# Optimization experiments

Measured on AMD Instinct MI355X. Metric: run time of the kernel, lower is better.

The kernel has to match this reference:

```python
import jax, jax.numpy as jnp
import numpy as np

EMBED_DIM = 768
NUM_HEADS = 12
HEAD_DIM = EMBED_DIM // NUM_HEADS
SCALE = HEAD_DIM ** -0.5


def setup_inputs() -> dict:
    key = jax.random.key(0)
    k_x, k_qkv, k_proj, k_pb = jax.random.split(key, 4)
    x = jax.random.normal(k_x, (2, 4096, EMBED_DIM), dtype=jnp.float32)
    # nn.Linear weights stored as [out, in]; qkv_bias=False -> no qkv bias
    W_qkv = jax.random.normal(k_qkv, (3 * EMBED_DIM, EMBED_DIM), dtype=jnp.float32) * (EMBED_DIM ** -0.5)
    W_proj = jax.random.normal(k_proj, (EMBED_DIM, EMBED_DIM), dtype=jnp.float32) * (EMBED_DIM ** -0.5)
    b_proj = jax.random.normal(k_pb, (EMBED_DIM,), dtype=jnp.float32) * 0.01
    return {"x": x, "W_qkv": W_qkv, "W_proj": W_proj, "b_proj": b_proj}


def reference(x, W_qkv, W_proj, b_proj):
    bs, seq_len, _ = x.shape
    qkv = jnp.einsum("bse,fe->bsf", x, W_qkv)  # [B,S,3E]
    q, k, v = jnp.split(qkv, 3, axis=-1)
    # [B,S,E] -> [B,H,S,D]
    def to_heads(t):
        return t.reshape(bs, seq_len, NUM_HEADS, HEAD_DIM).transpose(0, 2, 1, 3)
    q, k, v = to_heads(q), to_heads(k), to_heads(v)
    scores = jnp.einsum("bhqd,bhkd->bhqk", q, k) * SCALE
    attn = jax.nn.softmax(scores, axis=-1)  # dropout p=0.0 -> identity
    out = jnp.einsum("bhqk,bhkd->bhqd", attn, v)
    out = out.transpose(0, 2, 1, 3).reshape(bs, seq_len, EMBED_DIM)
    return jnp.einsum("bse,fe->bsf", out, W_proj) + b_proj
```

## Files before the change

kernel.cpp:

```cpp
#include <hip/hip_runtime.h>
#include <stdint.h>


typedef unsigned short u16;
typedef __attribute__((ext_vector_type(8))) short short8;
typedef __attribute__((ext_vector_type(4))) float float4v;

#define C2F 0.18033688011112042f

#if __has_builtin(__builtin_amdgcn_exp2f)
#define QSCALE C2F
#define FEXP(x) __builtin_amdgcn_exp2f(x)
#else
#define QSCALE 0.125f
#define FEXP(x) __expf(x)
#endif

__device__ __forceinline__ u16 f2bf(float f) {
  uint32_t u = __float_as_uint(f);
  u += 0x7FFFu + ((u >> 16) & 1u);
  return (u16)(u >> 16);
}
__device__ __forceinline__ float4v mfma16(short8 a, short8 b, float4v c) {
  return __builtin_amdgcn_mfma_f32_16x16x32_bf16(a, b, c, 0, 0, 0);
}
__device__ __forceinline__ short8 ld8(const u16* p) { return *(const short8*)p; }
__device__ __forceinline__ void st8(u16* p, short8 v) { *(short8*)p = v; }

__device__ __forceinline__ void dma16(const u16* g, u16* l) {
  __builtin_amdgcn_global_load_lds(
      (const __attribute__((address_space(1))) void*)g,
      (__attribute__((address_space(3))) void*)l, 16, 0, 0);
}

__device__ __forceinline__ uint32_t pk2(float lo, float hi) {
  return __builtin_amdgcn_perm(__float_as_uint(hi) + 0x8000u,
                               __float_as_uint(lo) + 0x8000u, 0x07060302u);
}
__device__ __forceinline__ short8 pack8(float4 a, float4 b) {
  union { short8 s; uint32_t u[4]; } r;
  r.u[0] = pk2(a.x, a.y); r.u[1] = pk2(a.z, a.w);
  r.u[2] = pk2(b.x, b.y); r.u[3] = pk2(b.z, b.w);
  return r.s;
}

__global__ __launch_bounds__(256, 3) void k_gemm_qkv(
    const float* __restrict__ x, const float* __restrict__ Wq,
    u16* __restrict__ qkv2, u16* __restrict__ Vt) {
  __shared__ u16 sA[128 * 64];
  __shared__ u16 sB[128 * 64];
  const int m0 = blockIdx.x * 128;
  const int f0 = blockIdx.y * 128;
  const bool vmode = (f0 >= 1536);
  const int tid = threadIdx.x;
  const int w = tid >> 6, lane = tid & 63;
  const int quad = lane >> 4, r = lane & 15;
  const int srow = lane >> 3, sc = lane & 7;

  float4v acc[4][4];
#pragma unroll
  for (int i = 0; i < 4; ++i)
#pragma unroll
    for (int j = 0; j < 4; ++j) acc[i][j] = (float4v){0.f, 0.f, 0.f, 0.f};

  float4 px[4][2], pw[4][2];
#pragma unroll
  for (int t = 0; t < 4; ++t) {
    const int row = 32 * w + 8 * t + srow;
    const float4* xa = (const float4*)x + (size_t)(m0 + row) * 192 + 2 * sc;
    const float4* wa = (const float4*)Wq + (size_t)(f0 + row) * 192 + 2 * sc;
    px[t][0] = xa[0]; px[t][1] = xa[1];
    pw[t][0] = wa[0]; pw[t][1] = wa[1];
  }

  for (int kt = 0; kt < 12; ++kt) {
#pragma unroll
    for (int t = 0; t < 4; ++t) {
      const int row = 32 * w + 8 * t + srow;
      st8(sA + row * 64 + 8 * (sc ^ srow), pack8(px[t][0], px[t][1]));
      st8(sB + row * 64 + 8 * (sc ^ srow), pack8(pw[t][0], pw[t][1]));
    }
    __syncthreads();
    if (kt + 1 < 12) {
#pragma unroll
      for (int t = 0; t < 4; ++t) {
        const int row = 32 * w + 8 * t + srow;
        const float4* xa = (const float4*)x + (size_t)(m0 + row) * 192 + (kt + 1) * 16 + 2 * sc;
        const float4* wa = (const float4*)Wq + (size_t)(f0 + row) * 192 + (kt + 1) * 16 + 2 * sc;
        px[t][0] = xa[0]; px[t][1] = xa[1];
        pw[t][0] = wa[0]; pw[t][1] = wa[1];
      }
    }
    const u16* At = vmode ? sB : sA;
    const u16* Bt = vmode ? sA : sB;
#pragma unroll
    for (int ks = 0; ks < 2; ++ks) {
      short8 a[4], b[4];
#pragma unroll
      for (int i = 0; i < 4; ++i) {
        const int ra = 64 * (w >> 1) + 16 * i + r;
        const int rb = 64 * (w & 1) + 16 * i + r;
        a[i] = ld8(At + ra * 64 + 8 * ((4 * ks + quad) ^ (ra & 7)));
        b[i] = ld8(Bt + rb * 64 + 8 * ((4 * ks + quad) ^ (rb & 7)));
      }
#pragma unroll
      for (int mi = 0; mi < 4; ++mi)
#pragma unroll
        for (int nf = 0; nf < 4; ++nf) acc[mi][nf] = mfma16(a[mi], b[nf], acc[mi][nf]);
    }
    __syncthreads();
  }

  if (!vmode) {
    const float qs = (f0 < 768) ? QSCALE : 1.0f;
#pragma unroll
    for (int mi = 0; mi < 4; ++mi) {
      const int m = m0 + 64 * (w >> 1) + 16 * mi + 4 * quad;
#pragma unroll
      for (int nf = 0; nf < 4; ++nf) {
        const int f = f0 + 64 * (w & 1) + 16 * nf + r;
#pragma unroll
        for (int reg = 0; reg < 4; ++reg)
          qkv2[(size_t)(m + reg) * 1536 + f] = f2bf(acc[mi][nf][reg] * qs);
      }
    }
  } else {
#pragma unroll
    for (int mi = 0; mi < 4; ++mi) {
      const int vcol = f0 - 1536 + 64 * (w >> 1) + 16 * mi + 4 * quad;
#pragma unroll
      for (int nf = 0; nf < 4; ++nf) {
        const int m = m0 + 64 * (w & 1) + 16 * nf + r;
        const int mp = (m & ~0x1C) | ((m & 0x0C) << 1) | ((m & 0x10) >> 2);
#pragma unroll
        for (int reg = 0; reg < 4; ++reg)
          Vt[(size_t)(vcol + reg) * 8192 + mp] = f2bf(acc[mi][nf][reg]);
      }
    }
  }
}

__global__ __launch_bounds__(512, 6) void k_flash(
    const u16* __restrict__ qkv2, const u16* __restrict__ Vt, u16* __restrict__ attn) {
  __shared__ u16 sK[2][64 * 64];
  __shared__ u16 sV[2][64 * 64];
  const int id = blockIdx.x;
  const int xcd = id & 7, slot = id >> 3;
  const int bh = xcd * 3 + (slot >> 5);
  const int qt = slot & 31;
  const int b = bh / 12, h = bh % 12;
  const int tid = threadIdx.x;
  const int w = tid >> 6, lane = tid & 63;
  const int quad = lane >> 4, r = lane & 15;
  const int srow = lane >> 3, sc = lane & 7;
  const u16* Qg = qkv2 + (size_t)b * 4096 * 1536 + h * 64;
  const u16* Kg = Qg + 768;
  const u16* Vg = Vt + (size_t)h * 64 * 8192 + (size_t)b * 4096;

  u16* sQ = &sK[0][0];
#pragma unroll
  for (int t = 0; t < 2; ++t) {
    const int row = 64 * t + (tid >> 3);
    st8(sQ + row * 64 + 8 * (sc ^ (row & 7)),
        ld8(Qg + (size_t)(qt * 128 + row) * 1536 + 8 * sc));
  }
  __syncthreads();
  short8 qf[2];
#pragma unroll
  for (int ks = 0; ks < 2; ++ks) {
    const int row = 16 * w + r;
    qf[ks] = ld8(sQ + row * 64 + 8 * ((4 * ks + quad) ^ (r & 7)));
  }
  __syncthreads();

  const int gsw = 8 * (sc ^ srow);
  const u16* kgp = Kg + (size_t)(8 * w + srow) * 1536 + gsw;
  const u16* vgp = Vg + (size_t)(8 * w + srow) * 8192 + gsw;
  const int ldso = w * 512;

  const int kfo0 = 64 * r + 8 * ((quad) ^ (r & 7));
  const int kfo1 = 64 * r + 8 * ((4 + quad) ^ (r & 7));
  const int pvoJ0 = 64 * r + 8 * ((0 + quad) ^ (r & 7));
  const int pvoJ1 = 64 * r + 8 * ((4 + quad) ^ (r & 7));

  const short8 ones8 = {0x3F80, 0x3F80, 0x3F80, 0x3F80,
                        0x3F80, 0x3F80, 0x3F80, 0x3F80};
  const float4v ZERO4 = {0.f, 0.f, 0.f, 0.f};
  float4v acc_l = ZERO4;
  float4v acc_o[4];
#pragma unroll
  for (int nf = 0; nf < 4; ++nf) acc_o[nf] = ZERO4;

  dma16(kgp, &sK[0][ldso]);
  dma16(vgp, &sV[0][ldso]);
  kgp += (size_t)64 * 1536;
  vgp += 64;

  int buf = 0;
  for (int kt = 0; kt < 64; ++kt) {
    __syncthreads();
    if (kt + 1 < 64) {
      const int nb = buf ^ 1;
      dma16(kgp, &sK[nb][ldso]);
      dma16(vgp, &sV[nb][ldso]);
      kgp += (size_t)64 * 1536;
      vgp += 64;
    }
    const u16* kb0 = &sK[buf][0] + kfo0;
    const u16* kb1 = &sK[buf][0] + kfo1;
    const u16* vb0 = &sV[buf][0];

    float4v s[4];
#pragma unroll
    for (int n4 = 0; n4 < 4; ++n4) {
      short8 kf = ld8(kb0 + 1024 * n4);
      s[n4] = mfma16(kf, qf[0], ZERO4);
    }
#pragma unroll
    for (int n4 = 0; n4 < 4; ++n4) {
      short8 kf = ld8(kb1 + 1024 * n4);
      s[n4] = mfma16(kf, qf[1], s[n4]);
    }

#pragma unroll
    for (int J = 0; J < 2; ++J) {
      union { short8 s8; uint32_t u[4]; } a;
#pragma unroll
      for (int h4 = 0; h4 < 2; ++h4) {
        const int n4 = 2 * J + h4;
#pragma unroll
        for (int reg = 0; reg < 4; ++reg) s[n4][reg] = FEXP(s[n4][reg]);
        a.u[2 * h4 + 0] = pk2(s[n4][0], s[n4][1]);
        a.u[2 * h4 + 1] = pk2(s[n4][2], s[n4][3]);
      }

      const u16* vbn = vb0 + (J ? pvoJ1 : pvoJ0);
#pragma unroll
      for (int nf = 0; nf < 4; ++nf) {
        short8 bv = ld8(vbn + 1024 * nf);
        acc_o[nf] = mfma16(a.s8, bv, acc_o[nf]);
      }
      acc_l = mfma16(a.s8, ones8, acc_l);
    }
    buf ^= 1;
  }

#pragma unroll
  for (int reg = 0; reg < 4; ++reg) {
    const float iv = 1.0f / acc_l[reg];
    const int q = qt * 128 + 16 * w + 4 * quad + reg;
#pragma unroll
    for (int nf = 0; nf < 4; ++nf)
      attn[(size_t)(b * 4096 + q) * 768 + h * 64 + 16 * nf + r] =
          f2bf(acc_o[nf][reg] * iv);
  }
}

__global__ __launch_bounds__(256, 3) void k_gemm_out(
    const u16* __restrict__ attn, const float* __restrict__ Wp,
    const float* __restrict__ bp, float* __restrict__ out) {
  __shared__ u16 sA[128 * 64];
  __shared__ u16 sB[128 * 64];
  const int m0 = blockIdx.x * 128;
  const int f0 = blockIdx.y * 128;
  const int tid = threadIdx.x;
  const int w = tid >> 6, lane = tid & 63;
  const int quad = lane >> 4, r = lane & 15;
  const int srow = lane >> 3, sc = lane & 7;

  float4v acc[4][4];
#pragma unroll
  for (int i = 0; i < 4; ++i)
#pragma unroll
    for (int j = 0; j < 4; ++j) acc[i][j] = (float4v){0.f, 0.f, 0.f, 0.f};

  short8 pa[4];
  float4 pw[4][2];
#pragma unroll
  for (int t = 0; t < 4; ++t) {
    const int row = 32 * w + 8 * t + srow;
    pa[t] = ld8(attn + (size_t)(m0 + row) * 768 + 8 * sc);
    const float4* wa = (const float4*)Wp + (size_t)(f0 + row) * 192 + 2 * sc;
    pw[t][0] = wa[0]; pw[t][1] = wa[1];
  }

  for (int kt = 0; kt < 12; ++kt) {
#pragma unroll
    for (int t = 0; t < 4; ++t) {
      const int row = 32 * w + 8 * t + srow;
      st8(sA + row * 64 + 8 * (sc ^ srow), pa[t]);
      st8(sB + row * 64 + 8 * (sc ^ srow), pack8(pw[t][0], pw[t][1]));
    }
    __syncthreads();
    if (kt + 1 < 12) {
#pragma unroll
      for (int t = 0; t < 4; ++t) {
        const int row = 32 * w + 8 * t + srow;
        pa[t] = ld8(attn + (size_t)(m0 + row) * 768 + (kt + 1) * 64 + 8 * sc);
        const float4* wa = (const float4*)Wp + (size_t)(f0 + row) * 192 + (kt + 1) * 16 + 2 * sc;
        pw[t][0] = wa[0]; pw[t][1] = wa[1];
      }
    }
#pragma unroll
    for (int ks = 0; ks < 2; ++ks) {
      short8 a[4], b[4];
#pragma unroll
      for (int i = 0; i < 4; ++i) {
        const int ra = 64 * (w >> 1) + 16 * i + r;
        const int rb = 64 * (w & 1) + 16 * i + r;
        a[i] = ld8(sA + ra * 64 + 8 * ((4 * ks + quad) ^ (ra & 7)));
        b[i] = ld8(sB + rb * 64 + 8 * ((4 * ks + quad) ^ (rb & 7)));
      }
#pragma unroll
      for (int mi = 0; mi < 4; ++mi)
#pragma unroll
        for (int nf = 0; nf < 4; ++nf) acc[mi][nf] = mfma16(a[mi], b[nf], acc[mi][nf]);
    }
    __syncthreads();
  }

#pragma unroll
  for (int mi = 0; mi < 4; ++mi) {
    const int m = m0 + 64 * (w >> 1) + 16 * mi + 4 * quad;
#pragma unroll
    for (int nf = 0; nf < 4; ++nf) {
      const int f = f0 + 64 * (w & 1) + 16 * nf + r;
      const float bias = bp[f];
#pragma unroll
      for (int reg = 0; reg < 4; ++reg)
        out[(size_t)(m + reg) * 768 + f] = acc[mi][nf][reg] + bias;
    }
  }
}

__global__ void k_copy(const uint4* __restrict__ src, uint4* __restrict__ dst, int n16) {
  int i = blockIdx.x * blockDim.x + threadIdx.x;
  if (i < n16) dst[i] = src[i];
}

extern "C" void kernel_launch(void* const* d_in, const int* in_sizes, int n_in,
                              void* d_out, int out_size, void* d_ws, size_t ws_size,
                              hipStream_t stream) {
  const float* x  = (const float*)d_in[0];
  const float* Wq = (const float*)d_in[1];
  const float* Wp = (const float*)d_in[2];
  const float* bp = (const float*)d_in[3];

  u16* qkv2 = (u16*)d_ws;
  u16* Vt   = qkv2 + (size_t)8192 * 1536;

  const bool big_ws = ws_size >= (size_t)48 * 1024 * 1024;
  u16* attn  = big_ws ? Vt + (size_t)768 * 8192 : (u16*)d_out;
  float* ogem = big_ws ? (float*)d_out : (float*)qkv2;

  hipLaunchKernelGGL(k_gemm_qkv, dim3(64, 18), dim3(256), 0, stream, x, Wq, qkv2, Vt);
  hipLaunchKernelGGL(k_flash, dim3(768), dim3(512), 0, stream, qkv2, Vt, attn);
  hipLaunchKernelGGL(k_gemm_out, dim3(64, 6), dim3(256), 0, stream, attn, Wp, bp, ogem);
  if (!big_ws) {
    const int n16 = (8192 * 768 * 4) / 16;
    hipLaunchKernelGGL(k_copy, dim3(n16 / 256), dim3(256), 0, stream,
                       (const uint4*)ogem, (uint4*)d_out, n16);
  }
}
```

Baseline: 268.9 us.

## Software-pipeline QK^T of next tile with softmax exp of current tile

Restructures the attention inner loop so the QK^T MFMAs for the next key tile are issued while the exp and bf16 packing of the current tile's scores run. K tiles are prefetched two iterations ahead, V tiles one ahead, and the K and V buffers are indexed separately. The aim is to hide transcendental and VALU latency behind matrix-core work. The cost is extra live registers for the in-flight scores, a prologue, and one wasted QK^T on stale data in the final iteration.

Result: faster. 257.9 us (-4.1%).

```diff
diff --git a/kernel.cpp b/kernel.cpp
--- a/kernel.cpp
+++ b/kernel.cpp
@@ -195,54 +195,67 @@
   dma16(vgp, &sV[0][ldso]);
   kgp += (size_t)64 * 1536;
   vgp += 64;
-
-  int buf = 0;
+  __syncthreads();
+
+  dma16(kgp, &sK[1][ldso]);
+  kgp += (size_t)64 * 1536;
+  float4v s[4];
+  {
+    const u16* kb0 = &sK[0][0] + kfo0;
+    const u16* kb1 = &sK[0][0] + kfo1;
+#pragma unroll
+    for (int n4 = 0; n4 < 4; ++n4) s[n4] = mfma16(ld8(kb0 + 1024 * n4), qf[0], ZERO4);
+#pragma unroll
+    for (int n4 = 0; n4 < 4; ++n4) s[n4] = mfma16(ld8(kb1 + 1024 * n4), qf[1], s[n4]);
+  }
+
+  int bufK = 0, bufV = 0;
   for (int kt = 0; kt < 64; ++kt) {
     __syncthreads();
-    if (kt + 1 < 64) {
-      const int nb = buf ^ 1;
-      dma16(kgp, &sK[nb][ldso]);
-      dma16(vgp, &sV[nb][ldso]);
-      kgp += (size_t)64 * 1536;
-      vgp += 64;
-    }
-    const u16* kb0 = &sK[buf][0] + kfo0;
-    const u16* kb1 = &sK[buf][0] + kfo1;
-    const u16* vb0 = &sV[buf][0];
-
-    float4v s[4];
-#pragma unroll
-    for (int n4 = 0; n4 < 4; ++n4) {
-      short8 kf = ld8(kb0 + 1024 * n4);
-      s[n4] = mfma16(kf, qf[0], ZERO4);
-    }
-#pragma unroll
-    for (int n4 = 0; n4 < 4; ++n4) {
-      short8 kf = ld8(kb1 + 1024 * n4);
-      s[n4] = mfma16(kf, qf[1], s[n4]);
-    }
-
-#pragma unroll
-    for (int J = 0; J < 2; ++J) {
-      union { short8 s8; uint32_t u[4]; } a;
-#pragma unroll
-      for (int h4 = 0; h4 < 2; ++h4) {
-        const int n4 = 2 * J + h4;
-#pragma unroll
-        for (int reg = 0; reg < 4; ++reg) s[n4][reg] = FEXP(s[n4][reg]);
-        a.u[2 * h4 + 0] = pk2(s[n4][0], s[n4][1]);
-        a.u[2 * h4 + 1] = pk2(s[n4][2], s[n4][3]);
-      }
-
-      const u16* vbn = vb0 + (J ? pvoJ1 : pvoJ0);
-#pragma unroll
-      for (int nf = 0; nf < 4; ++nf) {
-        short8 bv = ld8(vbn + 1024 * nf);
-        acc_o[nf] = mfma16(a.s8, bv, acc_o[nf]);
-      }
-      acc_l = mfma16(a.s8, ones8, acc_l);
-    }
-    buf ^= 1;
+    if (kt + 1 < 64) { dma16(vgp, &sV[bufV ^ 1][ldso]); vgp += 64; }
+    if (kt + 2 < 64) { dma16(kgp, &sK[bufK][ldso]); kgp += (size_t)64 * 1536; }
+
+    const u16* kb0 = &sK[bufK ^ 1][0] + kfo0;
+    const u16* kb1 = &sK[bufK ^ 1][0] + kfo1;
+    const u16* vb0 = &sV[bufV][0];
+
+    union { short8 s8; uint32_t u[4]; } a0, a1;
+#pragma unroll
+    for (int reg = 0; reg < 4; ++reg) {
+      s[0][reg] = FEXP(s[0][reg]);
+      s[1][reg] = FEXP(s[1][reg]);
+    }
+    a0.u[0] = pk2(s[0][0], s[0][1]); a0.u[1] = pk2(s[0][2], s[0][3]);
+    a0.u[2] = pk2(s[1][0], s[1][1]); a0.u[3] = pk2(s[1][2], s[1][3]);
+    float4v t0 = mfma16(ld8(kb0 + 1024 * 0), qf[0], ZERO4);
+    float4v t1 = mfma16(ld8(kb0 + 1024 * 1), qf[0], ZERO4);
+#pragma unroll
+    for (int reg = 0; reg < 4; ++reg) {
+      s[2][reg] = FEXP(s[2][reg]);
+      s[3][reg] = FEXP(s[3][reg]);
+    }
+    a1.u[0] = pk2(s[2][0], s[2][1]); a1.u[1] = pk2(s[2][2], s[2][3]);
+    a1.u[2] = pk2(s[3][0], s[3][1]); a1.u[3] = pk2(s[3][2], s[3][3]);
+    float4v t2 = mfma16(ld8(kb0 + 1024 * 2), qf[0], ZERO4);
+    float4v t3 = mfma16(ld8(kb0 + 1024 * 3), qf[0], ZERO4);
+    s[0] = mfma16(ld8(kb1 + 1024 * 0), qf[1], t0);
+    s[1] = mfma16(ld8(kb1 + 1024 * 1), qf[1], t1);
+    s[2] = mfma16(ld8(kb1 + 1024 * 2), qf[1], t2);
+    s[3] = mfma16(ld8(kb1 + 1024 * 3), qf[1], t3);
+
+    const u16* vJ0 = vb0 + pvoJ0;
+    const u16* vJ1 = vb0 + pvoJ1;
+#pragma unroll
+    for (int nf = 0; nf < 4; ++nf)
+      acc_o[nf] = mfma16(a0.s8, ld8(vJ0 + 1024 * nf), acc_o[nf]);
+    acc_l = mfma16(a0.s8, ones8, acc_l);
+#pragma unroll
+    for (int nf = 0; nf < 4; ++nf)
+      acc_o[nf] = mfma16(a1.s8, ld8(vJ1 + 1024 * nf), acc_o[nf]);
+    acc_l = mfma16(a1.s8, ones8, acc_l);
+
+    bufK ^= 1;
+    bufV ^= 1;
   }
 
 #pragma unroll
```
